# Optimization experiments

Measured on AMD Instinct MI355X. Metric: run time of the kernel, lower is better.

The kernel has to match this reference:

```python
import jax, jax.numpy as jnp
import numpy as np

INF = 1000000000000000.0  # 1e15, matches the TF source

B, H, S, D = 4, 16, 1024, 64


def setup_inputs() -> dict:
    key = jax.random.key(0)
    kq, kk, kv, kp = jax.random.split(key, 4)
    q = jax.random.normal(kq, (B, H, S, D), dtype=jnp.float32)
    k = jax.random.normal(kk, (B, H, S, D), dtype=jnp.float32)
    v = jax.random.normal(kv, (B, H, S, D), dtype=jnp.float32)
    # pad_mask: 1 = masked-out key position, broadcast over heads and queries
    pad_mask = jax.random.randint(kp, (B, 1, 1, S), 0, 2, dtype=jnp.int32)
    # look_ahead_mask: 1 above the diagonal (future positions masked)
    look_ahead_mask = jnp.triu(jnp.ones((S, S), dtype=jnp.int32), k=1)[None, None]
    return {"q": q, "k": k, "v": v, "pad_mask": pad_mask,
            "look_ahead_mask": look_ahead_mask}


def reference(q, k, v, pad_mask, look_ahead_mask):
    d_model = jnp.float32(q.shape[3])
    # scores: (B, H, Sq, Sk)
    score_logits = jnp.einsum("bhqd,bhkd->bhqk", q, k) / jnp.sqrt(d_model)
    if pad_mask is not None:
        score_logits = score_logits + pad_mask.astype(jnp.float32) * (-INF)
    if look_ahead_mask is not None:
        score_logits = score_logits + look_ahead_mask.astype(jnp.float32) * (-INF)
    attention_weights = jax.nn.softmax(score_logits, axis=-1)
    context_vector = jnp.einsum("bhqk,bhkd->bhqd", attention_weights, v)
    return (context_vector, attention_weights)
```

## Files before the change

### kernel.cpp

```cpp
#include <hip/hip_runtime.h>
#include <stdint.h>

#define S 1024
#define D 64
#define TQ 16
#define KT 256
#define NKT 4
#define NEG (-1e15f)
#define SCALE 0.125f

#define WB_STRIDE 1048
#define KB_STRIDE 72
#define VT_STRIDE 264
#define QS_STRIDE 72

typedef __bf16 bf16x8 __attribute__((ext_vector_type(8)));
typedef float f32x4 __attribute__((ext_vector_type(4)));
typedef unsigned short ushort_t;

__device__ __forceinline__ unsigned short f2b(float f) {
  union { float f; uint32_t u; } c; c.f = f;
  uint32_t u = c.u;
  return (unsigned short)((u + 0x7fffu + ((u >> 16) & 1u)) >> 16);
}
__device__ __forceinline__ float b2f(uint32_t u) {
  union { uint32_t u; float f; } c; c.u = u << 16;
  return c.f;
}

__global__ __launch_bounds__(256) void prep_k_kernel(
    const float* __restrict__ Kg, ushort_t* __restrict__ Kb)
{
  const size_t idx = ((size_t)blockIdx.x * 256 + threadIdx.x) * 8;
  float4 a = *(const float4*)(Kg + idx);
  float4 b = *(const float4*)(Kg + idx + 4);
  ushort_t tmp[8];
  tmp[0]=f2b(a.x); tmp[1]=f2b(a.y); tmp[2]=f2b(a.z); tmp[3]=f2b(a.w);
  tmp[4]=f2b(b.x); tmp[5]=f2b(b.y); tmp[6]=f2b(b.z); tmp[7]=f2b(b.w);
  *(uint4*)(Kb + idx) = *(const uint4*)tmp;
}

__global__ __launch_bounds__(256) void prep_vt_kernel(
    const float* __restrict__ Vg, ushort_t* __restrict__ Vt)
{
  __shared__ __align__(16) ushort_t lvt[D * QS_STRIDE];
  const int t = threadIdx.x;
  const int bh = blockIdx.x >> 4;
  const int j0 = (blockIdx.x & 15) << 6;

  {
    const int j = t >> 2, sd = (t & 3) << 4;
    const float* src = Vg + ((size_t)bh * S + j0 + j) * D + sd;
#pragma unroll
    for (int c = 0; c < 4; ++c) {
      float4 f = *(const float4*)(src + (c << 2));
      lvt[(sd + (c << 2) + 0) * QS_STRIDE + j] = f2b(f.x);
      lvt[(sd + (c << 2) + 1) * QS_STRIDE + j] = f2b(f.y);
      lvt[(sd + (c << 2) + 2) * QS_STRIDE + j] = f2b(f.z);
      lvt[(sd + (c << 2) + 3) * QS_STRIDE + j] = f2b(f.w);
    }
  }
  __syncthreads();
  {
    const int d = t >> 2, sj = (t & 3) << 4;
    ushort_t tmp[16];
#pragma unroll
    for (int c = 0; c < 4; ++c)
      *(ushort4*)&tmp[c << 2] = *(const ushort4*)&lvt[d * QS_STRIDE + sj + (c << 2)];
    ushort_t* dst = Vt + ((size_t)bh * D + d) * S + j0 + sj;
    *(uint4*)dst = *(const uint4*)&tmp[0];
    *(uint4*)(dst + 8) = *(const uint4*)&tmp[8];
  }
}

__global__ __launch_bounds__(512, 4) void attn_kernel(
    const float* __restrict__ Qg, const ushort_t* __restrict__ Kb,
    const ushort_t* __restrict__ Vtb, const int* __restrict__ PADg,
    float* __restrict__ OCTX, float* __restrict__ OW)
{
  __shared__ __align__(16) ushort_t wb[TQ * WB_STRIDE];
  __shared__ __align__(16) ushort_t ub[KT * KB_STRIDE];
  __shared__ __align__(16) ushort_t qs[TQ * QS_STRIDE];
  __shared__ __align__(16) float pbias[S];

  const int t  = threadIdx.x;
  const int w  = t >> 6;
  const int l  = t & 63;
  const int la = l & 15;
  const int lb = l >> 4;
  const int blk = blockIdx.x;
  const int bh  = blk >> 6;
  const int qt  = blk & 63;
  const int qr0 = qt << 4;

  const size_t head = (size_t)bh * S * D;

  if (t < 256) {
    const int r = t >> 4, c4 = (t & 15) << 2;
    const float4 qv = *(const float4*)(Qg + head + (size_t)(qr0 + r) * D + c4);
    ushort4 o; o.x = f2b(qv.x); o.y = f2b(qv.y); o.z = f2b(qv.z); o.w = f2b(qv.w);
    *(ushort4*)&qs[r * QS_STRIDE + c4] = o;
  } else {
    const int* pp = PADg + (size_t)(bh >> 4) * S;
    for (int j = t - 256; j < S; j += 256) pbias[j] = pp[j] ? NEG : 0.0f;
  }
  __syncthreads();

  const bf16x8 aq0 = *(const bf16x8*)&qs[la * QS_STRIDE +  0 + (lb << 3)];
  const bf16x8 aq1 = *(const bf16x8*)&qs[la * QS_STRIDE + 32 + (lb << 3)];

  for (int kt = 0; kt < NKT; ++kt) {
    {
      const ushort_t* kp = Kb + head + (size_t)(kt * KT) * D;
      const int row = t >> 1, half = (t & 1) << 5;
      const ushort_t* src = kp + row * D + half;
      ushort_t* dst = &ub[row * KB_STRIDE + half];
#pragma unroll
      for (int i = 0; i < 4; ++i)
        *(uint4*)(dst + (i << 3)) = *(const uint4*)(src + (i << 3));
    }
    __syncthreads();
#pragma unroll
    for (int sj = 0; sj < 2; ++sj) {
      const int j0 = (w << 5) + (sj << 4);
      f32x4 acc = {0.f, 0.f, 0.f, 0.f};
      bf16x8 b0 = *(const bf16x8*)&ub[(j0 + la) * KB_STRIDE +  0 + (lb << 3)];
      acc = __builtin_amdgcn_mfma_f32_16x16x32_bf16(aq0, b0, acc, 0, 0, 0);
      bf16x8 b1 = *(const bf16x8*)&ub[(j0 + la) * KB_STRIDE + 32 + (lb << 3)];
      acc = __builtin_amdgcn_mfma_f32_16x16x32_bf16(aq1, b1, acc, 0, 0, 0);
#pragma unroll
      for (int i = 0; i < 4; ++i)
        wb[((lb << 2) + i) * WB_STRIDE + kt * KT + j0 + la] = f2b(acc[i]);
    }
    __syncthreads();
  }

#pragma unroll
  for (int rr = 0; rr < 2; ++rr) {
    const int r  = (w << 1) + rr;
    const int qr = qr0 + r;
    float lg[16];
    float m = -3.0e38f;
#pragma unroll
    for (int ii = 0; ii < 8; ++ii) {
      const int j = (l << 1) + (ii << 7);
      uint32_t pr = *(const uint32_t*)&wb[r * WB_STRIDE + j];
      float2 pb = *(const float2*)&pbias[j];
      float l0 = b2f(pr & 0xffffu) * SCALE + pb.x + ((j     > qr) ? NEG : 0.0f);
      float l1 = b2f(pr >> 16)     * SCALE + pb.y + ((j + 1 > qr) ? NEG : 0.0f);
      lg[2 * ii] = l0; lg[2 * ii + 1] = l1;
      m = fmaxf(m, fmaxf(l0, l1));
    }
#pragma unroll
    for (int off = 32; off > 0; off >>= 1) m = fmaxf(m, __shfl_xor(m, off, 64));
    float sum = 0.f;
#pragma unroll
    for (int x = 0; x < 16; ++x) { lg[x] = __expf(lg[x] - m); sum += lg[x]; }
#pragma unroll
    for (int off = 32; off > 0; off >>= 1) sum += __shfl_xor(sum, off, 64);
    const float inv = 1.0f / sum;
    float* orow = OW + (size_t)(bh * S + qr) * S;
#pragma unroll
    for (int ii = 0; ii < 8; ++ii) {
      const int j = (l << 1) + (ii << 7);
      float w0 = lg[2 * ii] * inv, w1 = lg[2 * ii + 1] * inv;
      *(uint32_t*)&wb[r * WB_STRIDE + j] = ((uint32_t)f2b(w1) << 16) | (uint32_t)f2b(w0);
      *(float2*)&orow[j] = make_float2(w0, w1);
    }
  }
  __syncthreads();

  const int jh = w >> 2;
  const int d0 = (w & 3) << 4;
  f32x4 cacc = {0.f, 0.f, 0.f, 0.f};
  for (int kt = 0; kt < NKT; ++kt) {
    {
      const ushort_t* vp = Vtb + (size_t)bh * D * S + kt * KT;
      const int dd = t >> 3, seg = (t & 7) << 5;
      const ushort_t* src = vp + (size_t)dd * S + seg;
      ushort_t* dst = &ub[dd * VT_STRIDE + seg];
#pragma unroll
      for (int i = 0; i < 4; ++i)
        *(uint4*)(dst + (i << 3)) = *(const uint4*)(src + (i << 3));
    }
    __syncthreads();
#pragma unroll
    for (int ks = 0; ks < 4; ++ks) {
      const int jt = jh * 128 + ks * 32;
      bf16x8 af = *(const bf16x8*)&wb[la * WB_STRIDE + kt * KT + jt + (lb << 3)];
      bf16x8 bf = *(const bf16x8*)&ub[(d0 + la) * VT_STRIDE + jt + (lb << 3)];
      cacc = __builtin_amdgcn_mfma_f32_16x16x32_bf16(af, bf, cacc, 0, 0, 0);
    }
    __syncthreads();
  }

  float* pbuf = (float*)ub;
  if (w >= 4) {
#pragma unroll
    for (int i = 0; i < 4; ++i)
      pbuf[(w - 4) * 320 + ((lb << 2) + i) * 20 + la] = cacc[i];
  }
  __syncthreads();
  if (w < 4) {
#pragma unroll
    for (int i = 0; i < 4; ++i) {
      const int qrow = (lb << 2) + i;
      OCTX[((size_t)(bh * S) + qr0 + qrow) * D + d0 + la] =
          cacc[i] + pbuf[w * 320 + qrow * 20 + la];
    }
  }
}

extern "C" void kernel_launch(void* const* d_in, const int* in_sizes, int n_in,
                              void* d_out, int out_size, void* d_ws, size_t ws_size,
                              hipStream_t stream) {
  const float* q   = (const float*)d_in[0];
  const float* k   = (const float*)d_in[1];
  const float* v   = (const float*)d_in[2];
  const int*   pad = (const int*)d_in[3];
  float* ctx  = (float*)d_out;
  float* wout = (float*)d_out + (size_t)4 * 16 * S * D;

  ushort_t* Kb  = (ushort_t*)d_ws;
  ushort_t* Vtb = (ushort_t*)d_ws + (size_t)4 * 16 * S * D;

  prep_k_kernel <<<dim3(2048), dim3(256), 0, stream>>>(k, Kb);
  prep_vt_kernel<<<dim3(1024), dim3(256), 0, stream>>>(v, Vtb);
  attn_kernel   <<<dim3(4096), dim3(512), 0, stream>>>(q, Kb, Vtb, pad, ctx, wout);
}
```

Measured before the change: 413.9 us.

## Shrink LDS footprint: smaller K/V tiles, Q and pad mask read straight from global

Halves the K/V tile to 128 keys with twice as many tile iterations, and stops staging Q and the pad bias in shared memory. Q fragments are now loaded and converted per lane from global memory, and pad mask ints are read directly in the softmax loop. Launch bounds ask for 6 blocks per CU. The aim is lower LDS use and more resident blocks to hide memory latency, at the cost of twice as many barriers and redundant global reads of the mask. The epilogue reduction buffer (needs 4*320 floats) is still carved from ub, which is now 128*72 ushorts, roughly 18 KB, so it still fits.

```diff
diff --git a/kernel.cpp b/kernel.cpp
--- a/kernel.cpp
+++ b/kernel.cpp
@@ -4,14 +4,14 @@
 #define S 1024
 #define D 64
 #define TQ 16
-#define KT 256
-#define NKT 4
+#define KT 128
+#define NKT 8
 #define NEG (-1e15f)
 #define SCALE 0.125f
 
 #define WB_STRIDE 1048
 #define KB_STRIDE 72
-#define VT_STRIDE 264
+#define VT_STRIDE 136
 #define QS_STRIDE 72
 
 typedef __bf16 bf16x8 __attribute__((ext_vector_type(8)));
@@ -73,15 +73,13 @@
   }
 }
 
-__global__ __launch_bounds__(512, 4) void attn_kernel(
+__global__ __launch_bounds__(512, 6) void attn_kernel(
     const float* __restrict__ Qg, const ushort_t* __restrict__ Kb,
     const ushort_t* __restrict__ Vtb, const int* __restrict__ PADg,
     float* __restrict__ OCTX, float* __restrict__ OW)
 {
   __shared__ __align__(16) ushort_t wb[TQ * WB_STRIDE];
   __shared__ __align__(16) ushort_t ub[KT * KB_STRIDE];
-  __shared__ __align__(16) ushort_t qs[TQ * QS_STRIDE];
-  __shared__ __align__(16) float pbias[S];
 
   const int t  = threadIdx.x;
   const int w  = t >> 6;
@@ -94,37 +92,38 @@
   const int qr0 = qt << 4;
 
   const size_t head = (size_t)bh * S * D;
-
-  if (t < 256) {
-    const int r = t >> 4, c4 = (t & 15) << 2;
-    const float4 qv = *(const float4*)(Qg + head + (size_t)(qr0 + r) * D + c4);
-    ushort4 o; o.x = f2b(qv.x); o.y = f2b(qv.y); o.z = f2b(qv.z); o.w = f2b(qv.w);
-    *(ushort4*)&qs[r * QS_STRIDE + c4] = o;
-  } else {
-    const int* pp = PADg + (size_t)(bh >> 4) * S;
-    for (int j = t - 256; j < S; j += 256) pbias[j] = pp[j] ? NEG : 0.0f;
-  }
-  __syncthreads();
-
-  const bf16x8 aq0 = *(const bf16x8*)&qs[la * QS_STRIDE +  0 + (lb << 3)];
-  const bf16x8 aq1 = *(const bf16x8*)&qs[la * QS_STRIDE + 32 + (lb << 3)];
+  const int* pp = PADg + (size_t)(bh >> 4) * S;
+
+  bf16x8 aq0, aq1;
+  {
+    const float* qrow = Qg + head + (size_t)(qr0 + la) * D + (lb << 3);
+    float4 q00 = *(const float4*)(qrow);
+    float4 q01 = *(const float4*)(qrow + 4);
+    float4 q10 = *(const float4*)(qrow + 32);
+    float4 q11 = *(const float4*)(qrow + 36);
+    ushort_t a0[8], a1[8];
+    a0[0]=f2b(q00.x); a0[1]=f2b(q00.y); a0[2]=f2b(q00.z); a0[3]=f2b(q00.w);
+    a0[4]=f2b(q01.x); a0[5]=f2b(q01.y); a0[6]=f2b(q01.z); a0[7]=f2b(q01.w);
+    a1[0]=f2b(q10.x); a1[1]=f2b(q10.y); a1[2]=f2b(q10.z); a1[3]=f2b(q10.w);
+    a1[4]=f2b(q11.x); a1[5]=f2b(q11.y); a1[6]=f2b(q11.z); a1[7]=f2b(q11.w);
+    aq0 = *(const bf16x8*)a0;
+    aq1 = *(const bf16x8*)a1;
+  }
 
   for (int kt = 0; kt < NKT; ++kt) {
     {
       const ushort_t* kp = Kb + head + (size_t)(kt * KT) * D;
-      const int row = t >> 1, half = (t & 1) << 5;
-      const ushort_t* src = kp + row * D + half;
-      ushort_t* dst = &ub[row * KB_STRIDE + half];
-#pragma unroll
-      for (int i = 0; i < 4; ++i)
-        *(uint4*)(dst + (i << 3)) = *(const uint4*)(src + (i << 3));
-    }
-    __syncthreads();
-#pragma unroll
-    for (int sj = 0; sj < 2; ++sj) {
-      const int j0 = (w << 5) + (sj << 4);
+      const int row = t >> 2, off = (t & 3) << 4;
+      const ushort_t* src = kp + row * D + off;
+      ushort_t* dst = &ub[row * KB_STRIDE + off];
+      *(uint4*)dst = *(const uint4*)src;
+      *(uint4*)(dst + 8) = *(const uint4*)(src + 8);
+    }
+    __syncthreads();
+    {
+      const int j0 = w << 4;
       f32x4 acc = {0.f, 0.f, 0.f, 0.f};
-      bf16x8 b0 = *(const bf16x8*)&ub[(j0 + la) * KB_STRIDE +  0 + (lb << 3)];
+      bf16x8 b0 = *(const bf16x8*)&ub[(j0 + la) * KB_STRIDE + (lb << 3)];
       acc = __builtin_amdgcn_mfma_f32_16x16x32_bf16(aq0, b0, acc, 0, 0, 0);
       bf16x8 b1 = *(const bf16x8*)&ub[(j0 + la) * KB_STRIDE + 32 + (lb << 3)];
       acc = __builtin_amdgcn_mfma_f32_16x16x32_bf16(aq1, b1, acc, 0, 0, 0);
@@ -145,9 +144,9 @@
     for (int ii = 0; ii < 8; ++ii) {
       const int j = (l << 1) + (ii << 7);
       uint32_t pr = *(const uint32_t*)&wb[r * WB_STRIDE + j];
-      float2 pb = *(const float2*)&pbias[j];
-      float l0 = b2f(pr & 0xffffu) * SCALE + pb.x + ((j     > qr) ? NEG : 0.0f);
-      float l1 = b2f(pr >> 16)     * SCALE + pb.y + ((j + 1 > qr) ? NEG : 0.0f);
+      int2 pv = *(const int2*)&pp[j];
+      float l0 = b2f(pr & 0xffffu) * SCALE + (pv.x ? NEG : 0.0f) + ((j     > qr) ? NEG : 0.0f);
+      float l1 = b2f(pr >> 16)     * SCALE + (pv.y ? NEG : 0.0f) + ((j + 1 > qr) ? NEG : 0.0f);
       lg[2 * ii] = l0; lg[2 * ii + 1] = l1;
       m = fmaxf(m, fmaxf(l0, l1));
     }
@@ -176,17 +175,16 @@
   for (int kt = 0; kt < NKT; ++kt) {
     {
       const ushort_t* vp = Vtb + (size_t)bh * D * S + kt * KT;
-      const int dd = t >> 3, seg = (t & 7) << 5;
-      const ushort_t* src = vp + (size_t)dd * S + seg;
-      ushort_t* dst = &ub[dd * VT_STRIDE + seg];
-#pragma unroll
-      for (int i = 0; i < 4; ++i)
-        *(uint4*)(dst + (i << 3)) = *(const uint4*)(src + (i << 3));
-    }
-    __syncthreads();
-#pragma unroll
-    for (int ks = 0; ks < 4; ++ks) {
-      const int jt = jh * 128 + ks * 32;
+      const int dd = t >> 3, off = (t & 7) << 4;
+      const ushort_t* src = vp + (size_t)dd * S + off;
+      ushort_t* dst = &ub[dd * VT_STRIDE + off];
+      *(uint4*)dst = *(const uint4*)src;
+      *(uint4*)(dst + 8) = *(const uint4*)(src + 8);
+    }
+    __syncthreads();
+#pragma unroll
+    for (int ks = 0; ks < 2; ++ks) {
+      const int jt = jh * 64 + ks * 32;
       bf16x8 af = *(const bf16x8*)&wb[la * WB_STRIDE + kt * KT + jt + (lb << 3)];
       bf16x8 bf = *(const bf16x8*)&ub[(d0 + la) * VT_STRIDE + jt + (lb << 3)];
       cacc = __builtin_amdgcn_mfma_f32_16x16x32_bf16(af, bf, cacc, 0, 0, 0);
```

After: 409.7 us. About the same (-1.0%).
